# Kernel tuning notes

Hardware: AMD Instinct MI355X
Metric: run time of the kernel (lower is better)

The kernel has to match this reference:

```python
import jax, jax.numpy as jnp
import numpy as np

BITS = 4
MAXQ = 15          # (1 << BITS) - 1
PACK = 32 // BITS  # 8 values packed per int32


def dequantize(qweight, qzeros, scales, g_idx):
    """GPTQ 4-bit dequant. qweight: [K//8, N] int32, qzeros: [G, N//8] int32,
    scales: [G, N] float, g_idx: [K] int32 -> dense W [K, N] float."""
    N = qweight.shape[1]
    shifts = (jnp.arange(PACK, dtype=jnp.uint32) * BITS)  # [8]
    qw = qweight.astype(jnp.uint32)
    # unpack along K: k = row*8 + j  (matches shifter = (k % 8) * bits)
    w_int = ((qw[:, None, :] >> shifts[None, :, None]) & MAXQ).reshape(-1, N)  # [K, N]
    qz = qzeros.astype(jnp.uint32)
    # unpack along N: n = col*8 + j  (matches zeros_shifter = (n % 8) * bits)
    z_int = ((qz[:, :, None] >> shifts[None, None, :]) & MAXQ).reshape(qzeros.shape[0], -1) + 1  # [G, N]
    dt = scales.dtype
    # group-wise dequant: w = (q - zero) * scale, gathered per-row via g_idx
    return (w_int.astype(dt) - z_int[g_idx].astype(dt)) * scales[g_idx]


def setup_inputs() -> dict:
    key = jax.random.key(0)
    k1, k2, k3, k4, k5 = jax.random.split(key, 5)
    M, K, N, GS = 128, 4096, 11008, 128
    G = K // GS
    x = jax.random.normal(k1, (M, K), dtype=jnp.float32)
    qweight = jax.random.randint(k2, (K // PACK, N), 0, 2147483647, dtype=jnp.int32)
    qzeros = jax.random.randint(k3, (G, N // PACK), 0, 2147483647, dtype=jnp.int32)
    scales = jax.random.uniform(k4, (G, N), dtype=jnp.float32, minval=0.001, maxval=0.01)
    bias = jax.random.normal(k5, (N,), dtype=jnp.float32)
    g_idx = (jnp.arange(K, dtype=jnp.int32) // GS).astype(jnp.int32)
    return {"x": x, "qweight": qweight, "qzeros": qzeros, "scales": scales,
            "bias": bias, "g_idx": g_idx}


def reference(x, qweight, qzeros, scales, bias, g_idx):
    w = dequantize(qweight, qzeros, scales, g_idx)  # [K, N]
    return x @ w + bias
```

## Files before the change

### kernel.cpp

```cpp
#include <hip/hip_runtime.h>
#include <stdint.h>


#define M_DIM 128
#define K_DIM 4096
#define N_DIM 11008
#define GS    128
#define NG    32
#define SPLIT 4
#define GPB   (NG / SPLIT)
#define PART_STRIDE ((size_t)M_DIM * N_DIM)

typedef _Float16 half8  __attribute__((ext_vector_type(8)));
typedef _Float16 half2t __attribute__((ext_vector_type(2)));
typedef _Float16 half4t __attribute__((ext_vector_type(4)));
typedef float    f32x4  __attribute__((ext_vector_type(4)));

__global__ void k_prep(const float* __restrict__ x, const int* __restrict__ qzeros,
                       const float* __restrict__ scales,
                       _Float16* __restrict__ xh, float* __restrict__ zs) {
    int b = blockIdx.x, tid = threadIdx.x;
    if (b < 512) {
        int i = (b * 256 + tid) * 4;
        float4 v = *(const float4*)(x + i);
        half4t o;
        o[0] = (_Float16)v.x; o[1] = (_Float16)v.y;
        o[2] = (_Float16)v.z; o[3] = (_Float16)v.w;
        *(half4t*)(xh + i) = o;
    } else {
        b -= 512;
        int g = b / 43;
        int n = (b - g * 43) * 256 + tid;
        unsigned qz = (unsigned)qzeros[g * (N_DIM / 8) + (n >> 3)];
        float z = (float)((qz >> ((n & 7) * 4)) & 15u) + 1.0f;
        zs[g * N_DIM + n] = z * scales[g * N_DIM + n];
    }
}

__device__ __forceinline__ void load_lds16(const void* g, void* l) {
    __builtin_amdgcn_global_load_lds(
        (const __attribute__((address_space(1))) unsigned int*)g,
        (__attribute__((address_space(3))) unsigned int*)l, 16, 0, 0);
}

__device__ __forceinline__ half8 dequant8(unsigned q, half2t S2, half2t Z2) {
    const half2t BIAS = __builtin_bit_cast(half2t, 0x64006400u);
    half2t w[4];
#pragma unroll
    for (int p = 0; p < 4; ++p) {
        unsigned r = __builtin_amdgcn_perm(q, q, 0x00010001u * (unsigned)p);
        unsigned t = (r & 0x00F0000Fu) | 0x64006400u;
        w[p] = __builtin_elementwise_fma(__builtin_bit_cast(half2t, t) - BIAS, S2, Z2);
    }
    half4t lo = __builtin_shufflevector(w[0], w[1], 0, 1, 2, 3);
    half4t hi = __builtin_shufflevector(w[2], w[3], 0, 1, 2, 3);
    return __builtin_shufflevector(lo, hi, 0, 1, 2, 3, 4, 5, 6, 7);
}

__global__ __launch_bounds__(512, 4)
void k_gemm(const _Float16* __restrict__ xh,
            const int*      __restrict__ qweight,
            const float*    __restrict__ scales,
            const float*    __restrict__ zst,
            float*          __restrict__ part)
{
    __shared__ _Float16 As[2][128 * 128];

    const int tid  = threadIdx.x;
    const int lane = tid & 63;
    const int w    = tid >> 6;
    const int wx   = w & 1;
    const int wy   = (w >> 1) & 1;
    const int kh   = w >> 2;
    const int q    = lane >> 4;
    const int lr   = lane & 15;

    const int n0 = blockIdx.x * 64;
    const int g0 = blockIdx.y * GPB;
    int ncol[2] = { n0 + wx * 32 + lr, n0 + wx * 32 + lr + 16 };

    f32x4 acc[4][2];
#pragma unroll
    for (int f = 0; f < 4; ++f)
#pragma unroll
        for (int h = 0; h < 2; ++h)
            acc[f][h] = (f32x4){0.f, 0.f, 0.f, 0.f};

    int cm[4], ckb[4];
#pragma unroll
    for (int it = 0; it < 4; ++it) {
        int c = it * 512 + tid;
        cm[it]  = c >> 4;
        ckb[it] = (c & 15) ^ (cm[it] & 15);
    }
    const int wave_lds = w * 64 * 8;

#pragma unroll
    for (int it = 0; it < 4; ++it)
        load_lds16(xh + (size_t)cm[it] * K_DIM + g0 * GS + ckb[it] * 8,
                   &As[0][it * 512 * 8 + wave_lds]);
    unsigned qwn[4];
    float scn[2], zcn[2];
#pragma unroll
    for (int t = 0; t < 2; ++t)
#pragma unroll
        for (int h = 0; h < 2; ++h)
            qwn[t * 2 + h] = (unsigned)qweight[(size_t)(g0 * 16 + (kh * 2 + t) * 4 + q) * N_DIM + ncol[h]];
#pragma unroll
    for (int h = 0; h < 2; ++h) {
        scn[h] = scales[(size_t)g0 * N_DIM + ncol[h]];
        zcn[h] = zst[(size_t)g0 * N_DIM + ncol[h]];
    }

    int p = 0;
    for (int g = 0; g < GPB; ++g) {
        unsigned qw[4];
        float sc[2], zc[2];
#pragma unroll
        for (int i = 0; i < 4; ++i) qw[i] = qwn[i];
#pragma unroll
        for (int h = 0; h < 2; ++h) { sc[h] = scn[h]; zc[h] = zcn[h]; }

        __syncthreads();

        if (g + 1 < GPB) {
            int gn = g0 + g + 1;
#pragma unroll
            for (int it = 0; it < 4; ++it)
                load_lds16(xh + (size_t)cm[it] * K_DIM + gn * GS + ckb[it] * 8,
                           &As[p ^ 1][it * 512 * 8 + wave_lds]);
#pragma unroll
            for (int t = 0; t < 2; ++t)
#pragma unroll
                for (int h = 0; h < 2; ++h)
                    qwn[t * 2 + h] = (unsigned)qweight[(size_t)(gn * 16 + (kh * 2 + t) * 4 + q) * N_DIM + ncol[h]];
#pragma unroll
            for (int h = 0; h < 2; ++h) {
                scn[h] = scales[(size_t)gn * N_DIM + ncol[h]];
                zcn[h] = zst[(size_t)gn * N_DIM + ncol[h]];
            }
        }

        half2t S2[2], Z2[2];
#pragma unroll
        for (int h = 0; h < 2; ++h) {
            float s = sc[h], z1 = zc[h];
            S2[h][0] = (_Float16)s;
            S2[h][1] = (_Float16)(s * 0.0625f);
            Z2[h][0] = (_Float16)(-z1);
            Z2[h][1] = (_Float16)(-z1);
        }

#pragma unroll
        for (int t = 0; t < 2; ++t) {
            const int kk = kh * 2 + t;
            half8 bf[2];
#pragma unroll
            for (int h = 0; h < 2; ++h)
                bf[h] = dequant8(qw[t * 2 + h], S2[h], Z2[h]);
#pragma unroll
            for (int f = 0; f < 4; ++f) {
                int m   = wy * 64 + f * 16 + lr;
                int kb2 = (kk * 4 + q) ^ lr;
                half8 af = *(const half8*)(&As[p][m * 128 + kb2 * 8]);
#pragma unroll
                for (int h = 0; h < 2; ++h)
                    acc[f][h] = __builtin_amdgcn_mfma_f32_16x16x32_f16(af, bf[h], acc[f][h], 0, 0, 0);
            }
        }
        p ^= 1;
    }

    __syncthreads();
    float* red = (float*)&As[0][0];
    const int pid = w & 3;
    if (w >= 4) {
#pragma unroll
        for (int f = 0; f < 4; ++f)
#pragma unroll
            for (int h = 0; h < 2; ++h)
                *(f32x4*)(red + pid * 2048 + (f * 2 + h) * 256 + lane * 4) = acc[f][h];
    }
    __syncthreads();
    if (w < 4) {
        float* po = part + (size_t)blockIdx.y * PART_STRIDE;
#pragma unroll
        for (int f = 0; f < 4; ++f) {
            int mrow = wy * 64 + f * 16 + q * 4;
#pragma unroll
            for (int h = 0; h < 2; ++h) {
                f32x4 o = acc[f][h] + *(const f32x4*)(red + pid * 2048 + (f * 2 + h) * 256 + lane * 4);
#pragma unroll
                for (int r = 0; r < 4; ++r)
                    po[(size_t)(mrow + r) * N_DIM + ncol[h]] = o[r];
            }
        }
    }
}

__global__ void k_reduce(const float* __restrict__ part, const float* __restrict__ bias,
                         float* __restrict__ out) {
    int i = (blockIdx.x * 256 + threadIdx.x) * 4;
    int m = i / N_DIM;
    int n = i - m * N_DIM;
    f32x4 s = *(const f32x4*)(bias + n);
#pragma unroll
    for (int sp = 0; sp < SPLIT; ++sp)
        s += *(const f32x4*)(part + sp * PART_STRIDE + i);
    *(f32x4*)(out + i) = s;
}

extern "C" void kernel_launch(void* const* d_in, const int* in_sizes, int n_in,
                              void* d_out, int out_size, void* d_ws, size_t ws_size,
                              hipStream_t stream) {
    const float* x       = (const float*)d_in[0];
    const int*   qweight = (const int*)d_in[1];
    const int*   qzeros  = (const int*)d_in[2];
    const float* scales  = (const float*)d_in[3];
    const float* bias    = (const float*)d_in[4];

    char* ws = (char*)d_ws;
    _Float16* xh   = (_Float16*)ws;
    float*    zst  = (float*)(ws + 1048576);
    float*    part = (float*)(ws + 1048576 + 1409024);

    k_prep  <<<dim3(1888),            dim3(256), 0, stream>>>(x, qzeros, scales, xh, zst);
    k_gemm  <<<dim3(N_DIM/64, SPLIT), dim3(512), 0, stream>>>(xh, qweight, scales, zst, part);
    k_reduce<<<dim3(1376),            dim3(256), 0, stream>>>(part, bias, (float*)d_out);
}
```

Before: 103.6 us.

## Prefetch all group weights upfront and pack scale/zero into fp16 pairs

```diff
diff --git a/kernel.cpp b/kernel.cpp
--- a/kernel.cpp
+++ b/kernel.cpp
@@ -18,7 +18,7 @@
 
 __global__ void k_prep(const float* __restrict__ x, const int* __restrict__ qzeros,
                        const float* __restrict__ scales,
-                       _Float16* __restrict__ xh, float* __restrict__ zs) {
+                       _Float16* __restrict__ xh, half2t* __restrict__ zsc) {
     int b = blockIdx.x, tid = threadIdx.x;
     if (b < 512) {
         int i = (b * 256 + tid) * 4;
@@ -32,8 +32,12 @@
         int g = b / 43;
         int n = (b - g * 43) * 256 + tid;
         unsigned qz = (unsigned)qzeros[g * (N_DIM / 8) + (n >> 3)];
-        float z = (float)((qz >> ((n & 7) * 4)) & 15u) + 1.0f;
-        zs[g * N_DIM + n] = z * scales[g * N_DIM + n];
+        float z1 = (float)((qz >> ((n & 7) * 4)) & 15u) + 1.0f;
+        float s  = scales[g * N_DIM + n];
+        half2t o;
+        o[0] = (_Float16)s;
+        o[1] = (_Float16)(-z1 * s);
+        zsc[g * N_DIM + n] = o;
     }
 }
 
@@ -60,8 +64,7 @@
 __global__ __launch_bounds__(512, 4)
 void k_gemm(const _Float16* __restrict__ xh,
             const int*      __restrict__ qweight,
-            const float*    __restrict__ scales,
-            const float*    __restrict__ zst,
+            const half2t*   __restrict__ zsc,
             float*          __restrict__ part)
 {
     __shared__ _Float16 As[2][128 * 128];
@@ -99,28 +102,25 @@
     for (int it = 0; it < 4; ++it)
         load_lds16(xh + (size_t)cm[it] * K_DIM + g0 * GS + ckb[it] * 8,
                    &As[0][it * 512 * 8 + wave_lds]);
-    unsigned qwn[4];
-    float scn[2], zcn[2];
-#pragma unroll
-    for (int t = 0; t < 2; ++t)
+
+    unsigned qwA[GPB][4];
+    half2t   zs2[GPB][2];
+#pragma unroll
+    for (int gg = 0; gg < GPB; ++gg) {
+        int ga = g0 + gg;
+#pragma unroll
+        for (int t = 0; t < 2; ++t)
+#pragma unroll
+            for (int h = 0; h < 2; ++h)
+                qwA[gg][t * 2 + h] =
+                    (unsigned)qweight[(size_t)(ga * 16 + (kh * 2 + t) * 4 + q) * N_DIM + ncol[h]];
 #pragma unroll
         for (int h = 0; h < 2; ++h)
-            qwn[t * 2 + h] = (unsigned)qweight[(size_t)(g0 * 16 + (kh * 2 + t) * 4 + q) * N_DIM + ncol[h]];
-#pragma unroll
-    for (int h = 0; h < 2; ++h) {
-        scn[h] = scales[(size_t)g0 * N_DIM + ncol[h]];
-        zcn[h] = zst[(size_t)g0 * N_DIM + ncol[h]];
-    }
-
-    int p = 0;
+            zs2[gg][h] = zsc[(size_t)ga * N_DIM + ncol[h]];
+    }
+
+#pragma unroll
     for (int g = 0; g < GPB; ++g) {
-        unsigned qw[4];
-        float sc[2], zc[2];
-#pragma unroll
-        for (int i = 0; i < 4; ++i) qw[i] = qwn[i];
-#pragma unroll
-        for (int h = 0; h < 2; ++h) { sc[h] = scn[h]; zc[h] = zcn[h]; }
-
         __syncthreads();
 
         if (g + 1 < GPB) {
@@ -128,27 +128,16 @@
 #pragma unroll
             for (int it = 0; it < 4; ++it)
                 load_lds16(xh + (size_t)cm[it] * K_DIM + gn * GS + ckb[it] * 8,
-                           &As[p ^ 1][it * 512 * 8 + wave_lds]);
-#pragma unroll
-            for (int t = 0; t < 2; ++t)
-#pragma unroll
-                for (int h = 0; h < 2; ++h)
-                    qwn[t * 2 + h] = (unsigned)qweight[(size_t)(gn * 16 + (kh * 2 + t) * 4 + q) * N_DIM + ncol[h]];
-#pragma unroll
-            for (int h = 0; h < 2; ++h) {
-                scn[h] = scales[(size_t)gn * N_DIM + ncol[h]];
-                zcn[h] = zst[(size_t)gn * N_DIM + ncol[h]];
-            }
-        }
-
+                           &As[(g + 1) & 1][it * 512 * 8 + wave_lds]);
+        }
+
+        const half2t SC = { (_Float16)1.0f, (_Float16)0.0625f };
         half2t S2[2], Z2[2];
 #pragma unroll
         for (int h = 0; h < 2; ++h) {
-            float s = sc[h], z1 = zc[h];
-            S2[h][0] = (_Float16)s;
-            S2[h][1] = (_Float16)(s * 0.0625f);
-            Z2[h][0] = (_Float16)(-z1);
-            Z2[h][1] = (_Float16)(-z1);
+            half2t ss = __builtin_shufflevector(zs2[g][h], zs2[g][h], 0, 0);
+            S2[h] = ss * SC;
+            Z2[h] = __builtin_shufflevector(zs2[g][h], zs2[g][h], 1, 1);
         }
 
 #pragma unroll
@@ -157,18 +146,17 @@
             half8 bf[2];
 #pragma unroll
             for (int h = 0; h < 2; ++h)
-                bf[h] = dequant8(qw[t * 2 + h], S2[h], Z2[h]);
+                bf[h] = dequant8(qwA[g][t * 2 + h], S2[h], Z2[h]);
 #pragma unroll
             for (int f = 0; f < 4; ++f) {
                 int m   = wy * 64 + f * 16 + lr;
                 int kb2 = (kk * 4 + q) ^ lr;
-                half8 af = *(const half8*)(&As[p][m * 128 + kb2 * 8]);
+                half8 af = *(const half8*)(&As[g & 1][m * 128 + kb2 * 8]);
 #pragma unroll
                 for (int h = 0; h < 2; ++h)
                     acc[f][h] = __builtin_amdgcn_mfma_f32_16x16x32_f16(af, bf[h], acc[f][h], 0, 0, 0);
             }
         }
-        p ^= 1;
     }
 
     __syncthreads();
@@ -221,10 +209,10 @@
 
     char* ws = (char*)d_ws;
     _Float16* xh   = (_Float16*)ws;
-    float*    zst  = (float*)(ws + 1048576);
+    half2t*   zsc  = (half2t*)(ws + 1048576);
     float*    part = (float*)(ws + 1048576 + 1409024);
 
-    k_prep  <<<dim3(1888),            dim3(256), 0, stream>>>(x, qzeros, scales, xh, zst);
-    k_gemm  <<<dim3(N_DIM/64, SPLIT), dim3(512), 0, stream>>>(xh, qweight, scales, zst, part);
+    k_prep  <<<dim3(1888),            dim3(256), 0, stream>>>(x, qzeros, scales, xh, zsc);
+    k_gemm  <<<dim3(N_DIM/64, SPLIT), dim3(512), 0, stream>>>(xh, qweight, zsc, part);
     k_reduce<<<dim3(1376),            dim3(256), 0, stream>>>(part, bias, (float*)d_out);
 }
```

After: 105.2 us. No clear change (+1.6%).
